# Kernel optimization log

Hardware: AMD Instinct MI355X
Metric: run time of the kernel (lower is better)

The kernel has to match this reference:

```python
import jax, jax.numpy as jnp
import numpy as np

# config constants
H = 1024          # hidden_size
I = 512           # moe_intermediate_size
IS = 1024         # moe_shared_expert_intermediate_size
E = 16            # n_routed_experts
G = 4             # n_group
TOPK_G = 2        # topk_group
TOPK = 4          # num_experts_per_tok
SCALE = 2.5       # routed_scaling_factor
B, S = 2, 1024


def _relu2(x):
    r = jax.nn.relu(x)
    return r * r


def setup_inputs() -> dict:
    key = jax.random.key(0)
    ks = jax.random.split(key, 8)
    sd = 0.02
    return {
        "hidden_states": jax.random.normal(ks[0], (B, S, H), jnp.float32),
        "Wg": jax.random.normal(ks[1], (E, H), jnp.float32) * sd,          # router gate weight
        "bias_corr": jax.random.normal(ks[2], (E,), jnp.float32) * 0.01,    # e_score_correction_bias
        "W1": jax.random.normal(ks[3], (E, I, H), jnp.float32) * sd,        # experts up_proj
        "W2": jax.random.normal(ks[4], (E, H, I), jnp.float32) * sd,        # experts down_proj
        "Ws1": jax.random.normal(ks[5], (IS, H), jnp.float32) * sd,         # shared up_proj
        "Ws2": jax.random.normal(ks[6], (H, IS), jnp.float32) * sd,         # shared down_proj
    }


def _route(scores, bias_corr):
    # scores: (T,E) = sigmoid(router logits)
    T = scores.shape[0]
    s_choice = scores + bias_corr                                           # (T,E)
    gs = s_choice.reshape(T, G, E // G)
    group_scores = jnp.sum(jax.lax.top_k(gs, 2)[0], axis=-1)                # (T,G) sum of top-2 per group
    gidx = jax.lax.top_k(group_scores, TOPK_G)[1]                           # (T,topk_group)
    gmask = jnp.sum(jax.nn.one_hot(gidx, G, dtype=scores.dtype), axis=1)    # (T,G)
    smask = jnp.repeat(gmask, E // G, axis=1)                               # (T,E)
    masked = jnp.where(smask > 0, s_choice, 0.0)
    topk_idx = jax.lax.top_k(masked, TOPK)[1]                               # (T,top_k)
    topk_w = jnp.take_along_axis(scores, topk_idx, axis=1)                  # weights from raw sigmoid scores
    topk_w = topk_w / (jnp.sum(topk_w, axis=-1, keepdims=True) + 1e-20)     # norm_topk_prob
    topk_w = topk_w * SCALE
    return topk_idx, topk_w


def reference(hidden_states, Wg, bias_corr, W1, W2, Ws1, Ws2):
    b, s, h = hidden_states.shape
    flat = hidden_states.reshape(-1, h)                                     # (T,H)
    T = flat.shape[0]
    logits = flat.astype(jnp.float32) @ Wg.T                                # (T,E)
    scores = jax.nn.sigmoid(logits)
    topk_idx, topk_w = _route(scores, bias_corr)
    topk_w = topk_w.astype(hidden_states.dtype)
    # combined per-(token, expert) weight; zero where not routed (equivalent
    # to the per-expert gather/MLP/weighted index_add in the original)
    cw = jnp.zeros((T, E), flat.dtype)
    cw = cw.at[jnp.arange(T)[:, None], topk_idx].add(topk_w)                # (T,E)
    # fc1_latent_proj / fc2_latent_proj are Identity (moe_latent_size=None)
    hid = _relu2(jnp.einsum('th,eih->eti', flat, W1))                       # (E,T,I)
    y = jnp.einsum('eti,ehi->eth', hid, W2)                                 # (E,T,H)
    out = jnp.einsum('eth,te->th', y, cw)                                   # (T,H)
    shared = _relu2(flat @ Ws1.T) @ Ws2.T                                   # shared expert on residuals
    return (out + shared).reshape(b, s, h)
```

## Files before the change

kernel.cpp:

```cpp
#include <hip/hip_runtime.h>
#include <hip/hip_bf16.h>

#define T_TOK 2048
#define HDIM 1024
#define IDIM 512
#define ISDIM 1024
#define NEXP 16
#define TOPK 4
#define NSLOT (T_TOK*TOPK)
#define SCALE_F 2.5f

typedef unsigned short u16;
typedef float f32x4 __attribute__((ext_vector_type(4)));
typedef __bf16 bf16x8 __attribute__((ext_vector_type(8)));
typedef u16 u16x8 __attribute__((ext_vector_type(8)));

__device__ __forceinline__ u16 f2bf(float f) {
  unsigned u = __builtin_bit_cast(unsigned, f);
  u += 0x7fffu + ((u >> 16) & 1u);
  return (u16)(u >> 16);
}

__device__ __forceinline__ float bf2f(u16 h) {
  unsigned u = ((unsigned)h) << 16;
  return __builtin_bit_cast(float, u);
}

__device__ __forceinline__ void gload_lds16(const u16* g, u16* l) {
  __builtin_amdgcn_global_load_lds(
      (const __attribute__((address_space(1))) void*)g,
      (__attribute__((address_space(3))) void*)l, 16, 0, 0);
}

__device__ __forceinline__ f32x4 mfma16(u16x8 a, u16x8 b, f32x4 c) {
  return __builtin_amdgcn_mfma_f32_16x16x32_bf16(
      __builtin_bit_cast(bf16x8, a), __builtin_bit_cast(bf16x8, b), c, 0, 0, 0);
}

__global__ void __launch_bounds__(256) router_kernel(
    const float* __restrict__ x, const float* __restrict__ Wg,
    const float* __restrict__ bias,
    int* __restrict__ topk_idx, float* __restrict__ topk_w,
    u16* __restrict__ Xbf) {
  int t = blockIdx.x;
  int tid = threadIdx.x;
  int lane = tid & 63;
  int wave = tid >> 6;

  __shared__ __align__(16) float sx[HDIM];
  __shared__ float ssc[NEXP];

  float4 xv = reinterpret_cast<const float4*>(x + (size_t)t * HDIM)[tid];
  reinterpret_cast<float4*>(sx)[tid] = xv;
  ushort4 o;
  o.x = f2bf(xv.x); o.y = f2bf(xv.y); o.z = f2bf(xv.z); o.w = f2bf(xv.w);
  reinterpret_cast<ushort4*>(Xbf + (size_t)t * HDIM)[tid] = o;
  __syncthreads();

  float acc[4] = {0.f, 0.f, 0.f, 0.f};
  const float4* sx4 = reinterpret_cast<const float4*>(sx);
#pragma unroll
  for (int c = 0; c < 4; c++) {
    float4 xq = sx4[lane + 64 * c];
#pragma unroll
    for (int e = 0; e < 4; e++) {
      float4 wq = reinterpret_cast<const float4*>(
          Wg + (size_t)(wave * 4 + e) * HDIM)[lane + 64 * c];
      acc[e] += xq.x * wq.x + xq.y * wq.y + xq.z * wq.z + xq.w * wq.w;
    }
  }
#pragma unroll
  for (int e = 0; e < 4; e++) {
    float v = acc[e];
#pragma unroll
    for (int off = 32; off > 0; off >>= 1) v += __shfl_xor(v, off);
    if (lane == 0) ssc[wave * 4 + e] = v;
  }
  __syncthreads();

  if (tid == 0) {
    float scores[NEXP], sc[NEXP];
#pragma unroll
    for (int e = 0; e < NEXP; e++) {
      float s = 1.f / (1.f + expf(-ssc[e]));
      scores[e] = s;
      sc[e] = s + bias[e];
    }
    float gsum[4];
#pragma unroll
    for (int g = 0; g < 4; g++) {
      float a = sc[4*g], b = sc[4*g+1], c = sc[4*g+2], d = sc[4*g+3];
      float hi1 = fmaxf(a, b), lo1 = fminf(a, b);
      float hi2 = fmaxf(c, d), lo2 = fminf(c, d);
      gsum[g] = fmaxf(hi1, hi2) + fmaxf(fminf(hi1, hi2), fmaxf(lo1, lo2));
    }
    int g0 = 0; float bv = gsum[0];
#pragma unroll
    for (int g = 1; g < 4; g++) if (gsum[g] > bv) { bv = gsum[g]; g0 = g; }
    int g1 = -1; float bv2 = -1e30f;
#pragma unroll
    for (int g = 0; g < 4; g++) if (g != g0 && gsum[g] > bv2) { bv2 = gsum[g]; g1 = g; }
    float m[NEXP];
#pragma unroll
    for (int e = 0; e < NEXP; e++) {
      int g = e >> 2;
      m[e] = (g == g0 || g == g1) ? sc[e] : 0.0f;
    }
    int idx[TOPK]; float w[TOPK];
#pragma unroll
    for (int k = 0; k < TOPK; k++) {
      int bj = 0; float bmv = m[0];
#pragma unroll
      for (int j = 1; j < NEXP; j++) if (m[j] > bmv) { bmv = m[j]; bj = j; }
      idx[k] = bj; w[k] = scores[bj];
#pragma unroll
      for (int j = 0; j < NEXP; j++) m[j] = (j == bj) ? -1e30f : m[j];
    }
    float s4 = w[0] + w[1] + w[2] + w[3] + 1e-20f;
    float inv = SCALE_F / s4;
#pragma unroll
    for (int k = 0; k < TOPK; k++) {
      topk_idx[t * TOPK + k] = idx[k];
      topk_w[t * TOPK + k] = w[k] * inv;
    }
  }
}

__global__ void __launch_bounds__(256) route_build(
    const int* __restrict__ topk_idx, const float* __restrict__ topk_w,
    int* __restrict__ offsets, int* __restrict__ counts,
    int* __restrict__ perm_token, float* __restrict__ perm_w,
    int* __restrict__ slot_of) {
  __shared__ int hcnt[NEXP];
  __shared__ int hfill[NEXP];
  int tid = threadIdx.x;
  if (tid < NEXP) hcnt[tid] = 0;
  __syncthreads();

  int e_loc[NSLOT / 256];
#pragma unroll
  for (int i = 0; i < NSLOT / 256; i++) {
    int j = tid + 256 * i;
    int e = topk_idx[j];
    e_loc[i] = e;
    atomicAdd(&hcnt[e], 1);
  }
  __syncthreads();

  if (tid == 0) {
    int s = 0;
#pragma unroll
    for (int e = 0; e < NEXP; e++) {
      int c = hcnt[e];
      offsets[e] = s;
      counts[e] = c;
      hfill[e] = s;
      s += c;
    }
  }
  __syncthreads();

#pragma unroll
  for (int i = 0; i < NSLOT / 256; i++) {
    int j = tid + 256 * i;
    int pos = atomicAdd(&hfill[e_loc[i]], 1);
    perm_token[pos] = j >> 2;
    perm_w[pos] = topk_w[j];
    slot_of[j] = pos;
  }
}

#define N1Q (NEXP*IDIM*HDIM/4)
#define NSQ (ISDIM*HDIM/4)
__global__ void __launch_bounds__(256) cvt_all(
    const float* __restrict__ W1, const float* __restrict__ W2,
    const float* __restrict__ Ws1, const float* __restrict__ Ws2,
    u16* __restrict__ W1b, u16* __restrict__ W2b,
    u16* __restrict__ Ws1b, u16* __restrict__ Ws2b) {
  int i = blockIdx.x * 256 + threadIdx.x;
  const float* src; u16* dst; int off;
  if (i < N1Q)               { src = W1;  dst = W1b;  off = i; }
  else if (i < 2 * N1Q)      { src = W2;  dst = W2b;  off = i - N1Q; }
  else if (i < 2 * N1Q + NSQ){ src = Ws1; dst = Ws1b; off = i - 2 * N1Q; }
  else                       { src = Ws2; dst = Ws2b; off = i - 2 * N1Q - NSQ; }
  float4 v = reinterpret_cast<const float4*>(src)[off];
  ushort4 o;
  o.x = f2bf(v.x); o.y = f2bf(v.y); o.z = f2bf(v.z); o.w = f2bf(v.w);
  reinterpret_cast<ushort4*>(dst)[off] = o;
}

#define BM 64
#define BN 128
#define BK 64

template<int PHASE>
__global__ void __launch_bounds__(256) moe_gemm(
    const u16* __restrict__ Xbf, const u16* __restrict__ Hg,
    const u16* __restrict__ Hs,
    const u16* __restrict__ W1b, const u16* __restrict__ W2b,
    const u16* __restrict__ Ws1b, const u16* __restrict__ Ws2b,
    const int* __restrict__ eoffs, const int* __restrict__ ecnts,
    const int* __restrict__ rowmap, const float* __restrict__ rowscale,
    u16* __restrict__ HgOut, u16* __restrict__ HsOut,
    u16* __restrict__ Ygb, float* __restrict__ Ys)
{
  constexpr int KL = (PHASE == 0) ? HDIM : IDIM;

  int flat = blockIdx.x + gridDim.x * (blockIdx.y + gridDim.y * blockIdx.z);
  int chunk = (gridDim.x * gridDim.y * gridDim.z) >> 3;
  int widx = (flat & 7) * chunk + (flat >> 3);
  int mb = widx % gridDim.x;
  int tmp = widx / gridDim.x;
  int nb = tmp % gridDim.y;
  int e  = tmp / gridDim.y;

  bool sh = (e >= NEXP);
  int half = e - NEXP;
  int N, Mloc, rowbase, Astr, Bstr, kb;
  const u16* Abase;
  const u16* Bp;
  if (PHASE == 0) {
    Astr = HDIM; Bstr = HDIM; kb = 0;
    if (sh) { N = ISDIM; Mloc = T_TOK; rowbase = 0; Abase = Xbf; Bp = Ws1b; }
    else    { N = IDIM; Mloc = ecnts[e]; rowbase = eoffs[e]; Abase = Xbf;
              Bp = W1b + (size_t)e * IDIM * HDIM; }
  } else {
    N = HDIM;
    if (sh) { Astr = ISDIM; Bstr = ISDIM; kb = half * IDIM;
              Mloc = T_TOK; rowbase = 0; Abase = Hs; Bp = Ws2b; }
    else    { Astr = IDIM; Bstr = IDIM; kb = 0;
              Mloc = ecnts[e]; rowbase = eoffs[e]; Abase = Hg;
              Bp = W2b + (size_t)e * HDIM * IDIM; }
  }
  int m0 = mb * BM;
  if (m0 >= Mloc) return;
  int n0 = nb * BN;
  if (n0 >= N) return;

  __shared__ __align__(16) u16 sA[BM * BK];
  __shared__ __align__(16) u16 sB[BN * BK];

  int tid = threadIdx.x;
  int lane = tid & 63;
  int wave = tid >> 6;
  int wm = (wave >> 1) * 32;
  int wn = (wave & 1) * 64;
  int fm = lane & 15;
  int kq = lane >> 4;
  int fsw = fm & 7;

  int lrow8 = lane >> 3;
  int sch = ((lane & 7) ^ lrow8) * 8;

  const u16* AgP[2];
  u16* sAw[2];
#pragma unroll
  for (int g = 0; g < 2; g++) {
    int rt = 16 * wave + 8 * g + lrow8;
    int ar = m0 + rt;
    int arc = (ar < Mloc) ? ar : (Mloc - 1);
    size_t asrc;
    if (PHASE == 0 && !sh) asrc = (size_t)rowmap[rowbase + arc] * Astr;
    else                   asrc = (size_t)((sh ? 0 : rowbase) + arc) * Astr;
    AgP[g] = Abase + asrc + kb + sch;
    sAw[g] = &sA[(16 * wave + 8 * g) * BK];
  }
  const u16* BgP[4];
  u16* sBw[4];
#pragma unroll
  for (int g = 0; g < 4; g++) {
    int rt = 32 * wave + 8 * g + lrow8;
    BgP[g] = Bp + (size_t)(n0 + rt) * Bstr + kb + sch;
    sBw[g] = &sB[(32 * wave + 8 * g) * BK];
  }

  f32x4 acc[2][4] = {};

  for (int k0 = 0; k0 < KL; k0 += BK) {
#pragma unroll
    for (int g = 0; g < 2; g++) gload_lds16(AgP[g] + k0, sAw[g]);
#pragma unroll
    for (int g = 0; g < 4; g++) gload_lds16(BgP[g] + k0, sBw[g]);
    __syncthreads();
#pragma unroll
    for (int ks = 0; ks < 2; ks++) {
      int ch = ((ks * 4 + kq) ^ fsw) * 8;
      u16x8 af[2], bf[4];
#pragma unroll
      for (int i = 0; i < 2; i++)
        af[i] = *reinterpret_cast<const u16x8*>(&sA[(wm + 16 * i + fm) * BK + ch]);
#pragma unroll
      for (int j = 0; j < 4; j++)
        bf[j] = *reinterpret_cast<const u16x8*>(&sB[(wn + 16 * j + fm) * BK + ch]);
#pragma unroll
      for (int i = 0; i < 2; i++)
#pragma unroll
        for (int j = 0; j < 4; j++)
          acc[i][j] = mfma16(af[i], bf[j], acc[i][j]);
    }
    __syncthreads();
  }

#pragma unroll
  for (int i = 0; i < 2; i++) {
#pragma unroll
    for (int j = 0; j < 4; j++) {
      int gn = n0 + wn + 16 * j + fm;
      f32x4 a = acc[i][j];
#pragma unroll
      for (int r = 0; r < 4; r++) {
        int gm = m0 + wm + 16 * i + kq * 4 + r;
        if (gm < Mloc) {
          float v = a[r];
          if (PHASE == 0) {
            float tq = fmaxf(v, 0.f);
            if (!sh) {
              tq = tq * tq * rowscale[rowbase + gm];
              HgOut[(size_t)(rowbase + gm) * IDIM + gn] = f2bf(tq);
            } else {
              HsOut[(size_t)gm * ISDIM + gn] = f2bf(tq * tq);
            }
          } else {
            if (!sh) Ygb[(size_t)(rowbase + gm) * HDIM + gn] = f2bf(v);
            else     Ys[(size_t)(half * T_TOK + gm) * HDIM + gn] = v;
          }
        }
      }
    }
  }
}

__global__ void __launch_bounds__(256) combine_kernel(
    const u16* __restrict__ Ygb, const float* __restrict__ Ys,
    const int* __restrict__ slot_of, float* __restrict__ out) {
  int t = blockIdx.x;
  int i = threadIdx.x;
  int4 s = *reinterpret_cast<const int4*>(&slot_of[t * 4]);
  const ushort4* Y4 = reinterpret_cast<const ushort4*>(Ygb);
  const float4* S4 = reinterpret_cast<const float4*>(Ys);
  float4* O4 = reinterpret_cast<float4*>(out);
  float4 v0 = S4[(size_t)t * 256 + i];
  float4 v1 = S4[(size_t)(T_TOK + t) * 256 + i];
  ushort4 a = Y4[(size_t)s.x * 256 + i];
  ushort4 b = Y4[(size_t)s.y * 256 + i];
  ushort4 c = Y4[(size_t)s.z * 256 + i];
  ushort4 d = Y4[(size_t)s.w * 256 + i];
  float4 v;
  v.x = v0.x + v1.x + bf2f(a.x) + bf2f(b.x) + bf2f(c.x) + bf2f(d.x);
  v.y = v0.y + v1.y + bf2f(a.y) + bf2f(b.y) + bf2f(c.y) + bf2f(d.y);
  v.z = v0.z + v1.z + bf2f(a.z) + bf2f(b.z) + bf2f(c.z) + bf2f(d.z);
  v.w = v0.w + v1.w + bf2f(a.w) + bf2f(b.w) + bf2f(c.w) + bf2f(d.w);
  O4[(size_t)t * 256 + i] = v;
}

extern "C" void kernel_launch(void* const* d_in, const int* in_sizes, int n_in,
                              void* d_out, int out_size, void* d_ws, size_t ws_size,
                              hipStream_t stream) {
  const float* x    = (const float*)d_in[0];
  const float* Wg   = (const float*)d_in[1];
  const float* bias = (const float*)d_in[2];
  const float* W1   = (const float*)d_in[3];
  const float* W2   = (const float*)d_in[4];
  const float* Ws1  = (const float*)d_in[5];
  const float* Ws2  = (const float*)d_in[6];
  float* out = (float*)d_out;

  char* p = (char*)d_ws;
  auto alloc = [&](size_t bytes) -> void* {
    void* r = (void*)p;
    p += (bytes + 255) & ~(size_t)255;
    return r;
  };
  int*   topk_idx   = (int*)  alloc((size_t)NSLOT * 4);
  float* topk_w     = (float*)alloc((size_t)NSLOT * 4);
  int*   counts     = (int*)  alloc(64);
  int*   offsets    = (int*)  alloc(64);
  int*   perm_token = (int*)  alloc((size_t)NSLOT * 4);
  float* perm_w     = (float*)alloc((size_t)NSLOT * 4);
  int*   slot_of    = (int*)  alloc((size_t)NSLOT * 4);
  u16*   Xbf        = (u16*)  alloc((size_t)T_TOK * HDIM * 2);
  u16*   W1b        = (u16*)  alloc((size_t)NEXP * IDIM * HDIM * 2);
  u16*   W2b        = (u16*)  alloc((size_t)NEXP * HDIM * IDIM * 2);
  u16*   Ws1b      = (u16*)  alloc((size_t)ISDIM * HDIM * 2);
  u16*   Ws2b      = (u16*)  alloc((size_t)HDIM * ISDIM * 2);
  u16*   Hg         = (u16*)  alloc((size_t)NSLOT * IDIM * 2);
  u16*   Hs         = (u16*)  alloc((size_t)T_TOK * ISDIM * 2);
  u16*   Ygb        = (u16*)  alloc((size_t)NSLOT * HDIM * 2);
  float* Ys         = (float*)alloc((size_t)2 * T_TOK * HDIM * 4);

  router_kernel<<<T_TOK, 256, 0, stream>>>(x, Wg, bias, topk_idx, topk_w, Xbf);
  route_build<<<1, 256, 0, stream>>>(topk_idx, topk_w, offsets, counts,
                                     perm_token, perm_w, slot_of);

  cvt_all<<<(2 * N1Q + 2 * NSQ + 255) / 256, 256, 0, stream>>>(
      W1, W2, Ws1, Ws2, W1b, W2b, Ws1b, Ws2b);

  moe_gemm<0><<<dim3(T_TOK / BM, ISDIM / BN, NEXP + 1), 256, 0, stream>>>(
      Xbf, Hg, Hs, W1b, W2b, Ws1b, Ws2b, offsets, counts,
      perm_token, perm_w, Hg, Hs, nullptr, nullptr);

  moe_gemm<1><<<dim3(T_TOK / BM, HDIM / BN, NEXP + 2), 256, 0, stream>>>(
      Xbf, Hg, Hs, W1b, W2b, Ws1b, Ws2b, offsets, counts,
      perm_token, perm_w, Hg, Hs, Ygb, Ys);

  combine_kernel<<<T_TOK, 256, 0, stream>>>(Ygb, Ys, slot_of, out);
}
```

Measured before the change: 249.8 us.

## Double-buffer LDS tiles and enlarge M tile to 128 in MoE GEMM

Doubles the M tile per block from 64 to 128 rows, so each wave computes a 4x4 grid of MFMA tiles and reuses each B fragment twice as often. LDS tiles are now double-buffered: the next K slice is prefetched into the alternate buffer while the current one is computed, removing one barrier per iteration. The epilogue is reordered so the row scale is loaded once per row. The cost is more registers and LDS per block and fewer blocks, so lightly loaded experts waste more of the larger M tile.

```diff
diff --git a/kernel.cpp b/kernel.cpp
--- a/kernel.cpp
+++ b/kernel.cpp
@@ -189,7 +189,7 @@
   reinterpret_cast<ushort4*>(dst)[off] = o;
 }
 
-#define BM 64
+#define BM 128
 #define BN 128
 #define BK 64
 
@@ -237,13 +237,13 @@
   int n0 = nb * BN;
   if (n0 >= N) return;
 
-  __shared__ __align__(16) u16 sA[BM * BK];
-  __shared__ __align__(16) u16 sB[BN * BK];
+  __shared__ __align__(16) u16 sA[2][BM * BK];
+  __shared__ __align__(16) u16 sB[2][BN * BK];
 
   int tid = threadIdx.x;
   int lane = tid & 63;
   int wave = tid >> 6;
-  int wm = (wave >> 1) * 32;
+  int wm = (wave >> 1) * 64;
   int wn = (wave & 1) * 64;
   int fm = lane & 15;
   int kq = lane >> 4;
@@ -252,70 +252,81 @@
   int lrow8 = lane >> 3;
   int sch = ((lane & 7) ^ lrow8) * 8;
 
-  const u16* AgP[2];
-  u16* sAw[2];
-#pragma unroll
-  for (int g = 0; g < 2; g++) {
-    int rt = 16 * wave + 8 * g + lrow8;
+  const u16* AgP[4];
+  int aoff[4];
+#pragma unroll
+  for (int g = 0; g < 4; g++) {
+    int rt = 32 * wave + 8 * g + lrow8;
     int ar = m0 + rt;
     int arc = (ar < Mloc) ? ar : (Mloc - 1);
     size_t asrc;
     if (PHASE == 0 && !sh) asrc = (size_t)rowmap[rowbase + arc] * Astr;
     else                   asrc = (size_t)((sh ? 0 : rowbase) + arc) * Astr;
     AgP[g] = Abase + asrc + kb + sch;
-    sAw[g] = &sA[(16 * wave + 8 * g) * BK];
+    aoff[g] = (32 * wave + 8 * g) * BK;
   }
   const u16* BgP[4];
-  u16* sBw[4];
+  int boff[4];
 #pragma unroll
   for (int g = 0; g < 4; g++) {
     int rt = 32 * wave + 8 * g + lrow8;
     BgP[g] = Bp + (size_t)(n0 + rt) * Bstr + kb + sch;
-    sBw[g] = &sB[(32 * wave + 8 * g) * BK];
-  }
-
-  f32x4 acc[2][4] = {};
-
+    boff[g] = (32 * wave + 8 * g) * BK;
+  }
+
+  f32x4 acc[4][4] = {};
+
+#pragma unroll
+  for (int g = 0; g < 4; g++) gload_lds16(AgP[g], &sA[0][aoff[g]]);
+#pragma unroll
+  for (int g = 0; g < 4; g++) gload_lds16(BgP[g], &sB[0][boff[g]]);
+  __syncthreads();
+
+  int cur = 0;
   for (int k0 = 0; k0 < KL; k0 += BK) {
-#pragma unroll
-    for (int g = 0; g < 2; g++) gload_lds16(AgP[g] + k0, sAw[g]);
-#pragma unroll
-    for (int g = 0; g < 4; g++) gload_lds16(BgP[g] + k0, sBw[g]);
-    __syncthreads();
+    int nxt = cur ^ 1;
+    if (k0 + BK < KL) {
+#pragma unroll
+      for (int g = 0; g < 4; g++) gload_lds16(AgP[g] + k0 + BK, &sA[nxt][aoff[g]]);
+#pragma unroll
+      for (int g = 0; g < 4; g++) gload_lds16(BgP[g] + k0 + BK, &sB[nxt][boff[g]]);
+    }
 #pragma unroll
     for (int ks = 0; ks < 2; ks++) {
       int ch = ((ks * 4 + kq) ^ fsw) * 8;
-      u16x8 af[2], bf[4];
-#pragma unroll
-      for (int i = 0; i < 2; i++)
-        af[i] = *reinterpret_cast<const u16x8*>(&sA[(wm + 16 * i + fm) * BK + ch]);
+      u16x8 af[4], bf[4];
+#pragma unroll
+      for (int i = 0; i < 4; i++)
+        af[i] = *reinterpret_cast<const u16x8*>(&sA[cur][(wm + 16 * i + fm) * BK + ch]);
 #pragma unroll
       for (int j = 0; j < 4; j++)
-        bf[j] = *reinterpret_cast<const u16x8*>(&sB[(wn + 16 * j + fm) * BK + ch]);
-#pragma unroll
-      for (int i = 0; i < 2; i++)
+        bf[j] = *reinterpret_cast<const u16x8*>(&sB[cur][(wn + 16 * j + fm) * BK + ch]);
+#pragma unroll
+      for (int i = 0; i < 4; i++)
 #pragma unroll
         for (int j = 0; j < 4; j++)
           acc[i][j] = mfma16(af[i], bf[j], acc[i][j]);
     }
     __syncthreads();
-  }
-
-#pragma unroll
-  for (int i = 0; i < 2; i++) {
-#pragma unroll
-    for (int j = 0; j < 4; j++) {
-      int gn = n0 + wn + 16 * j + fm;
-      f32x4 a = acc[i][j];
-#pragma unroll
-      for (int r = 0; r < 4; r++) {
-        int gm = m0 + wm + 16 * i + kq * 4 + r;
-        if (gm < Mloc) {
-          float v = a[r];
+    cur = nxt;
+  }
+
+#pragma unroll
+  for (int i = 0; i < 4; i++) {
+#pragma unroll
+    for (int r = 0; r < 4; r++) {
+      int gm = m0 + wm + 16 * i + kq * 4 + r;
+      if (gm < Mloc) {
+        float rs = 0.f;
+        if (PHASE == 0 && !sh) rs = rowscale[rowbase + gm];
+#pragma unroll
+        for (int j = 0; j < 4; j++) {
+          int gn = n0 + wn + 16 * j + fm;
+          float v = acc[i][j][r];
           if (PHASE == 0) {
             float tq = fmaxf(v, 0.f);
             if (!sh) {
-              tq = tq * tq * rowscale[rowbase + gm];
+              tq = tq * tq * rs;
               HgOut[(size_t)(rowbase + gm) * IDIM + gn] = f2bf(tq);
             } else {
               HsOut[(size_t)gm * ISDIM + gn] = f2bf(tq * tq);
```

Measured after the change: 284.2 us. 13.8% more time.

## Double-buffer LDS tiles in MoE GEMM with async prefetch two stages ahead

Applied to the files above, without the earlier changes.

Converts the single-buffered GEMM main loop into a two-stage LDS ping-pong. Global-to-LDS loads for tile t+2 are issued while MFMAs run on tile t, with explicit vmcnt/lgkmcnt waits and barriers. Fragments are read into registers before the buffer is overwritten, so load latency is hidden behind compute. The epilogue is also reordered so the rowscale load is hoisted per row. This doubles LDS use, which may lower occupancy, and relies on hand-tuned waitcnt values being correct.

```diff
diff --git a/kernel.cpp b/kernel.cpp
--- a/kernel.cpp
+++ b/kernel.cpp
@@ -36,6 +36,10 @@
   return __builtin_amdgcn_mfma_f32_16x16x32_bf16(
       __builtin_bit_cast(bf16x8, a), __builtin_bit_cast(bf16x8, b), c, 0, 0, 0);
 }
+
+__device__ __forceinline__ void wait_vm6()   { asm volatile("s_waitcnt vmcnt(6)" ::: "memory"); }
+__device__ __forceinline__ void wait_vm0()   { asm volatile("s_waitcnt vmcnt(0)" ::: "memory"); }
+__device__ __forceinline__ void wait_lgkm0() { asm volatile("s_waitcnt lgkmcnt(0)" ::: "memory"); }
 
 __global__ void __launch_bounds__(256) router_kernel(
     const float* __restrict__ x, const float* __restrict__ Wg,
@@ -205,6 +209,7 @@
     u16* __restrict__ Ygb, float* __restrict__ Ys)
 {
   constexpr int KL = (PHASE == 0) ? HDIM : IDIM;
+  constexpr int NT = KL / BK;
 
   int flat = blockIdx.x + gridDim.x * (blockIdx.y + gridDim.y * blockIdx.z);
   int chunk = (gridDim.x * gridDim.y * gridDim.z) >> 3;
@@ -237,8 +242,8 @@
   int n0 = nb * BN;
   if (n0 >= N) return;
 
-  __shared__ __align__(16) u16 sA[BM * BK];
-  __shared__ __align__(16) u16 sB[BN * BK];
+  __shared__ __align__(16) u16 sA[2][BM * BK];
+  __shared__ __align__(16) u16 sB[2][BN * BK];
 
   int tid = threadIdx.x;
   int lane = tid & 63;
@@ -253,7 +258,7 @@
   int sch = ((lane & 7) ^ lrow8) * 8;
 
   const u16* AgP[2];
-  u16* sAw[2];
+  int aoff[2];
 #pragma unroll
   for (int g = 0; g < 2; g++) {
     int rt = 16 * wave + 8 * g + lrow8;
@@ -263,59 +268,102 @@
     if (PHASE == 0 && !sh) asrc = (size_t)rowmap[rowbase + arc] * Astr;
     else                   asrc = (size_t)((sh ? 0 : rowbase) + arc) * Astr;
     AgP[g] = Abase + asrc + kb + sch;
-    sAw[g] = &sA[(16 * wave + 8 * g) * BK];
+    aoff[g] = (16 * wave + 8 * g) * BK;
   }
   const u16* BgP[4];
-  u16* sBw[4];
+  int boff[4];
 #pragma unroll
   for (int g = 0; g < 4; g++) {
     int rt = 32 * wave + 8 * g + lrow8;
     BgP[g] = Bp + (size_t)(n0 + rt) * Bstr + kb + sch;
-    sBw[g] = &sB[(32 * wave + 8 * g) * BK];
+    boff[g] = (32 * wave + 8 * g) * BK;
   }
 
   f32x4 acc[2][4] = {};
 
-  for (int k0 = 0; k0 < KL; k0 += BK) {
-#pragma unroll
-    for (int g = 0; g < 2; g++) gload_lds16(AgP[g] + k0, sAw[g]);
-#pragma unroll
-    for (int g = 0; g < 4; g++) gload_lds16(BgP[g] + k0, sBw[g]);
-    __syncthreads();
+#pragma unroll
+  for (int g = 0; g < 2; g++) gload_lds16(AgP[g], &sA[0][aoff[g]]);
+#pragma unroll
+  for (int g = 0; g < 4; g++) gload_lds16(BgP[g], &sB[0][boff[g]]);
+#pragma unroll
+  for (int g = 0; g < 2; g++) gload_lds16(AgP[g] + BK, &sA[1][aoff[g]]);
+#pragma unroll
+  for (int g = 0; g < 4; g++) gload_lds16(BgP[g] + BK, &sB[1][boff[g]]);
+
+  for (int t = 0; t < NT - 1; ++t) {
+    int cur = t & 1;
+    wait_vm6();
+    __builtin_amdgcn_s_barrier();
+    u16x8 af[2][2], bf[2][4];
 #pragma unroll
     for (int ks = 0; ks < 2; ks++) {
       int ch = ((ks * 4 + kq) ^ fsw) * 8;
-      u16x8 af[2], bf[4];
 #pragma unroll
       for (int i = 0; i < 2; i++)
-        af[i] = *reinterpret_cast<const u16x8*>(&sA[(wm + 16 * i + fm) * BK + ch]);
+        af[ks][i] = *reinterpret_cast<const u16x8*>(&sA[cur][(wm + 16 * i + fm) * BK + ch]);
 #pragma unroll
       for (int j = 0; j < 4; j++)
-        bf[j] = *reinterpret_cast<const u16x8*>(&sB[(wn + 16 * j + fm) * BK + ch]);
+        bf[ks][j] = *reinterpret_cast<const u16x8*>(&sB[cur][(wn + 16 * j + fm) * BK + ch]);
+    }
+    wait_lgkm0();
+    __builtin_amdgcn_sched_barrier(0);
+    __builtin_amdgcn_s_barrier();
+    if (t + 2 < NT) {
+#pragma unroll
+      for (int g = 0; g < 2; g++) gload_lds16(AgP[g] + (t + 2) * BK, &sA[cur][aoff[g]]);
+#pragma unroll
+      for (int g = 0; g < 4; g++) gload_lds16(BgP[g] + (t + 2) * BK, &sB[cur][boff[g]]);
+    }
+#pragma unroll
+    for (int ks = 0; ks < 2; ks++)
 #pragma unroll
       for (int i = 0; i < 2; i++)
 #pragma unroll
         for (int j = 0; j < 4; j++)
-          acc[i][j] = mfma16(af[i], bf[j], acc[i][j]);
-    }
-    __syncthreads();
+          acc[i][j] = mfma16(af[ks][i], bf[ks][j], acc[i][j]);
+  }
+  {
+    constexpr int cur = (NT - 1) & 1;
+    wait_vm0();
+    __builtin_amdgcn_s_barrier();
+    u16x8 af[2][2], bf[2][4];
+#pragma unroll
+    for (int ks = 0; ks < 2; ks++) {
+      int ch = ((ks * 4 + kq) ^ fsw) * 8;
+#pragma unroll
+      for (int i = 0; i < 2; i++)
+        af[ks][i] = *reinterpret_cast<const u16x8*>(&sA[cur][(wm + 16 * i + fm) * BK + ch]);
+#pragma unroll
+      for (int j = 0; j < 4; j++)
+        bf[ks][j] = *reinterpret_cast<const u16x8*>(&sB[cur][(wn + 16 * j + fm) * BK + ch]);
+    }
+    wait_lgkm0();
+    __builtin_amdgcn_sched_barrier(0);
+#pragma unroll
+    for (int ks = 0; ks < 2; ks++)
+#pragma unroll
+      for (int i = 0; i < 2; i++)
+#pragma unroll
+        for (int j = 0; j < 4; j++)
+          acc[i][j] = mfma16(af[ks][i], bf[ks][j], acc[i][j]);
   }
 
 #pragma unroll
   for (int i = 0; i < 2; i++) {
 #pragma unroll
-    for (int j = 0; j < 4; j++) {
-      int gn = n0 + wn + 16 * j + fm;
-      f32x4 a = acc[i][j];
-#pragma unroll
-      for (int r = 0; r < 4; r++) {
-        int gm = m0 + wm + 16 * i + kq * 4 + r;
-        if (gm < Mloc) {
-          float v = a[r];
+    for (int r = 0; r < 4; r++) {
+      int gm = m0 + wm + 16 * i + kq * 4 + r;
+      if (gm < Mloc) {
+        float rs = 0.f;
+        if (PHASE == 0 && !sh) rs = rowscale[rowbase + gm];
+#pragma unroll
+        for (int j = 0; j < 4; j++) {
+          int gn = n0 + wn + 16 * j + fm;
+          float v = acc[i][j][r];
           if (PHASE == 0) {
             float tq = fmaxf(v, 0.f);
             if (!sh) {
-              tq = tq * tq * rowscale[rowbase + gm];
+              tq = tq * tq * rs;
               HgOut[(size_t)(rowbase + gm) * IDIM + gn] = f2bf(tq);
             } else {
               HsOut[(size_t)gm * ISDIM + gn] = f2bf(tq * tq);
```

Result: slower. 257.3 us (+3.0%).
